# Kernel optimization log

Measured on AMD Instinct MI355X. Metric: run time of the kernel, lower is better.

The kernel has to match this reference:

```python
import jax, jax.numpy as jnp
import numpy as np

B, N1, N2, C = 4, 1024, 128, 1152
H, D = 16, 72            # num_heads, head_dim (1152 = 16*72)
HID = 4608               # mlp hidden = 4*1152
ATTN_SCALE = D ** -0.5
RMS_SCALE = C ** 0.5     # quirk: RMSNorm built with dim=1152 though applied over d=72
LN_EPS = 1e-6


def setup_inputs() -> dict:
    key = jax.random.key(0)
    ks = iter(jax.random.split(key, 64))
    n = lambda shape, s=1.0: jax.random.normal(next(ks), shape, jnp.float32) * s
    W = 0.02  # weight init scale
    inp = {
        "x": n((B, N1, C)),
        "c": n((B, N2, C)),
        "global_c": n((B, C)),
        "ada_x_w": n((C, 6 * C), W), "ada_x_b": jnp.zeros((6 * C,)),
        "ada_c_w": n((C, 6 * C), W), "ada_c_b": jnp.zeros((6 * C,)),
        "g1x_g": jnp.ones((C,)), "g1x_b": jnp.zeros((C,)),
        "g2x_g": jnp.ones((C,)), "g2x_b": jnp.zeros((C,)),
        "g1c_g": jnp.ones((C,)), "g1c_b": jnp.zeros((C,)),
        "g2c_g": jnp.ones((C,)), "g2c_b": jnp.zeros((C,)),
        "qkv_x_w": n((C, 3 * C), W), "qkv_x_b": jnp.zeros((3 * C,)),
        "proj_x_w": n((C, C), W), "proj_x_b": jnp.zeros((C,)),
        "qkv_c_w": n((C, 3 * C), W), "qkv_c_b": jnp.zeros((3 * C,)),
        "proj_c_w": n((C, C), W), "proj_c_b": jnp.zeros((C,)),
        "gq_x": jnp.ones((1,)), "gk_x": jnp.ones((1,)),
        "gq_c": jnp.ones((1,)), "gk_c": jnp.ones((1,)),
        "mlp_x_w1": n((C, HID), W), "mlp_x_b1": jnp.zeros((HID,)),
        "mlp_x_w2": n((HID, C), W), "mlp_x_b2": jnp.zeros((C,)),
        "mlp_c_w1": n((C, HID), W), "mlp_c_b1": jnp.zeros((HID,)),
        "mlp_c_w2": n((HID, C), W), "mlp_c_b2": jnp.zeros((C,)),
    }
    return inp


def _ln(t, g, b):
    m = t.mean(-1, keepdims=True)
    v = ((t - m) ** 2).mean(-1, keepdims=True)
    return (t - m) * jax.lax.rsqrt(v + LN_EPS) * g + b


def _modulate(t, shift, scale):  # shift/scale: [B, C]
    return t * (1.0 + scale[:, None, :]) + shift[:, None, :]


def _rms(t, g):  # F.normalize over last dim, then * sqrt(1152) * g
    nrm = jnp.sqrt(jnp.sum(t * t, axis=-1, keepdims=True))
    return t / jnp.maximum(nrm, 1e-12) * (RMS_SCALE * g)


def _heads(t):  # [B, N, H*D] -> [B, H, N, D]
    Bq, Nq, _ = t.shape
    return t.reshape(Bq, Nq, H, D).transpose(0, 2, 1, 3)


def _mmdit_forward(x, c, global_c,
                   ada_x_w, ada_x_b, ada_c_w, ada_c_b,
                   g1x_g, g1x_b, g2x_g, g2x_b, g1c_g, g1c_b, g2c_g, g2c_b,
                   qkv_x_w, qkv_x_b, proj_x_w, proj_x_b,
                   qkv_c_w, qkv_c_b, proj_c_w, proj_c_b,
                   gq_x, gk_x, gq_c, gk_c,
                   mlp_x_w1, mlp_x_b1, mlp_x_w2, mlp_x_b2,
                   mlp_c_w1, mlp_c_b1, mlp_c_w2, mlp_c_b2):
    s = jax.nn.silu(global_c)
    mod_x = jnp.split(s @ ada_x_w + ada_x_b, 6, axis=-1)
    mod_c = jnp.split(s @ ada_c_w + ada_c_b, 6, axis=-1)
    (sh_msa_x, sc_msa_x, gt_msa_x, sh_mlp_x, sc_mlp_x, gt_mlp_x) = mod_x
    (sh_msa_c, sc_msa_c, gt_msa_c, sh_mlp_c, sc_mlp_c, gt_mlp_c) = mod_c

    xin = _modulate(_ln(x, g1x_g, g1x_b), sh_msa_x, sc_msa_x)
    cin = _modulate(_ln(c, g1c_g, g1c_b), sh_msa_c, sc_msa_c)

    qx, kx, vx = jnp.split(xin @ qkv_x_w + qkv_x_b, 3, axis=-1)
    qc, kc, vc = jnp.split(cin @ qkv_c_w + qkv_c_b, 3, axis=-1)
    qx, kx, vx = _heads(qx), _heads(kx), _heads(vx)
    qc, kc, vc = _heads(qc), _heads(kc), _heads(vc)
    qx, kx = _rms(qx, gq_x), _rms(kx, gk_x)
    qc, kc = _rms(qc, gq_c), _rms(kc, gk_c)

    q = jnp.concatenate([qx, qc], axis=2)  # [B,H,N1+N2,D]
    k = jnp.concatenate([kx, kc], axis=2)
    v = jnp.concatenate([vx, vc], axis=2)

    scores = jnp.einsum('bhnd,bhmd->bhnm', q, k) * ATTN_SCALE
    attn = jax.nn.softmax(scores, axis=-1)
    o = jnp.einsum('bhnm,bhmd->bhnd', attn, v)
    o = o.transpose(0, 2, 1, 3).reshape(B, N1 + N2, C)
    ox, oc = o[:, :N1], o[:, N1:]
    attn_x = ox @ proj_x_w + proj_x_b
    attn_c = oc @ proj_c_w + proj_c_b

    x = x + gt_msa_x[:, None, :] * attn_x
    c = c + gt_msa_c[:, None, :] * attn_c

    hx = _modulate(_ln(x, g2x_g, g2x_b), sh_mlp_x, sc_mlp_x)
    hx = jax.nn.gelu(hx @ mlp_x_w1 + mlp_x_b1, approximate=True) @ mlp_x_w2 + mlp_x_b2
    x = x + gt_mlp_x[:, None, :] * hx

    hc = _modulate(_ln(c, g2c_g, g2c_b), sh_mlp_c, sc_mlp_c)
    hc = jax.nn.gelu(hc @ mlp_c_w1 + mlp_c_b1, approximate=True) @ mlp_c_w2 + mlp_c_b2
    c = c + gt_mlp_c[:, None, :] * hc
    return x, c


def reference(x, c, global_c,
              ada_x_w, ada_x_b, ada_c_w, ada_c_b,
              g1x_g, g1x_b, g2x_g, g2x_b, g1c_g, g1c_b, g2c_g, g2c_b,
              qkv_x_w, qkv_x_b, proj_x_w, proj_x_b,
              qkv_c_w, qkv_c_b, proj_c_w, proj_c_b,
              gq_x, gk_x, gq_c, gk_c,
              mlp_x_w1, mlp_x_b1, mlp_x_w2, mlp_x_b2,
              mlp_c_w1, mlp_c_b1, mlp_c_w2, mlp_c_b2):
    return _mmdit_forward(x, c, global_c,
                          ada_x_w, ada_x_b, ada_c_w, ada_c_b,
                          g1x_g, g1x_b, g2x_g, g2x_b, g1c_g, g1c_b, g2c_g, g2c_b,
                          qkv_x_w, qkv_x_b, proj_x_w, proj_x_b,
                          qkv_c_w, qkv_c_b, proj_c_w, proj_c_b,
                          gq_x, gk_x, gq_c, gk_c,
                          mlp_x_w1, mlp_x_b1, mlp_x_w2, mlp_x_b2,
                          mlp_c_w1, mlp_c_b1, mlp_c_w2, mlp_c_b2)
```

## Files before the change

### kernel.cpp

```cpp
#include <hip/hip_runtime.h>

typedef unsigned short u16;
typedef unsigned int u32;
typedef __attribute__((ext_vector_type(8))) short bf16x8;
typedef __attribute__((ext_vector_type(4))) float f32x4;

#define MX_ 4096
#define NT_ 1152
#define C_  1152
#define DP_ 96
#define D_  72
#define H_  16
#define MT_ 4608

static __device__ __forceinline__ float b2f(u16 u){ union{u32 i; float f;} x; x.i=((u32)u)<<16; return x.f; }
static __device__ __forceinline__ u16 f2b(float f){ u32 i=__float_as_uint(f); return (u16)((i + 0x7FFFu + ((i>>16)&1u))>>16); }

static __device__ __forceinline__ void gl_lds16(const u16* g, u16* l){
  __builtin_amdgcn_global_load_lds((const __attribute__((address_space(1))) void*)g,
                                   (__attribute__((address_space(3))) void*)l, 16, 0, 0);
}

#define MFMA16(a,b,c) __builtin_amdgcn_mfma_f32_16x16x32_bf16(a,b,c,0,0,0)

struct TrArgs {
  const float* src[8]; u16* dst[8]; int K[8]; int N[8]; int start[9];
};

__global__ __launch_bounds__(256) void transpose_kernel(TrArgs a){
  int bx = blockIdx.x;
  int mi = 0;
  #pragma unroll
  for (int i = 0; i < 8; ++i) if (bx >= a.start[i+1]) mi = i+1;
  int t = bx - a.start[mi];
  int K = a.K[mi], N = a.N[mi];
  int ntk = K >> 5;
  int tk = t % ntk, tn = t / ntk;
  int k0 = tk*32, n0 = tn*32;
  __shared__ u16 lds[32][33];
  int c = threadIdx.x & 31, r = threadIdx.x >> 5;
  const float* src = a.src[mi];
  u16* dst = a.dst[mi];
  #pragma unroll
  for (int ii = 0; ii < 4; ++ii){
    int row = r + ii*8;
    lds[row][c] = f2b(src[(size_t)(k0+row)*N + n0 + c]);
  }
  __syncthreads();
  #pragma unroll
  for (int ii = 0; ii < 4; ++ii){
    int row = r + ii*8;
    dst[(size_t)(n0+row)*K + k0 + c] = lds[c][row];
  }
}

__global__ __launch_bounds__(256) void ada_kernel(const float* gc, const float* wx, const float* bx,
                                                  const float* wc, const float* bc,
                                                  float* mod_x, float* mod_c){
  __shared__ float s[4][C_];
  __shared__ float part[4][4][64];
  int tid = threadIdx.x;
  for (int i = tid; i < 4*C_; i += 256){
    float v = gc[i];
    s[i / C_][i % C_] = v / (1.f + __expf(-v));
  }
  __syncthreads();
  int jq = tid & 63;
  int kq = tid >> 6;
  int jg = blockIdx.x*64 + jq;
  int which = jg / 6912;
  int j = jg % 6912;
  const float* W = which ? wc : wx;
  float a0=0.f, a1=0.f, a2=0.f, a3=0.f;
  for (int k = kq*288; k < kq*288 + 288; ++k){
    float w = W[(size_t)k*6912 + j];
    a0 += s[0][k]*w; a1 += s[1][k]*w; a2 += s[2][k]*w; a3 += s[3][k]*w;
  }
  part[kq][0][jq]=a0; part[kq][1][jq]=a1; part[kq][2][jq]=a2; part[kq][3][jq]=a3;
  __syncthreads();
  if (kq == 0){
    float bb = (which ? bc : bx)[j];
    float* out = which ? mod_c : mod_x;
    #pragma unroll
    for (int b = 0; b < 4; ++b){
      out[(size_t)b*6912 + j] = part[0][b][jq] + part[1][b][jq] + part[2][b][jq] + part[3][b][jq] + bb;
    }
  }
}

__global__ __launch_bounds__(256) void ln_mod_kernel(
  const float* srcx, const float* srcc, const float* g, const float* bt,
  const float* gcn, const float* btc,
  const float* shx, const float* scx, const float* shc, const float* scc,
  u16* out)
{
  int m = blockIdx.x;
  bool isC = (m >= MX_);
  const float* src = isC ? srcc + (size_t)(m - MX_)*C_ : srcx + (size_t)m*C_;
  int bidx = isC ? ((m - MX_) >> 7) : (m >> 10);
  const float* gg = isC ? gcn : g;
  const float* bb = isC ? btc : bt;
  const float* sh = (isC ? shc : shx) + (size_t)bidx*6912;
  const float* sc = (isC ? scc : scx) + (size_t)bidx*6912;
  int tid = threadIdx.x;
  float lv[8];
  float sum = 0.f, sq = 0.f;
  if (tid < 144){
    float4 v0 = *(const float4*)(src + tid*8);
    float4 v1 = *(const float4*)(src + tid*8 + 4);
    lv[0]=v0.x; lv[1]=v0.y; lv[2]=v0.z; lv[3]=v0.w;
    lv[4]=v1.x; lv[5]=v1.y; lv[6]=v1.z; lv[7]=v1.w;
    #pragma unroll
    for (int j = 0; j < 8; ++j){ sum += lv[j]; sq += lv[j]*lv[j]; }
  }
  #pragma unroll
  for (int off = 1; off < 64; off <<= 1){ sum += __shfl_xor(sum, off); sq += __shfl_xor(sq, off); }
  __shared__ float rs[4], rq[4];
  int wave = tid >> 6, lane = tid & 63;
  if (lane == 0){ rs[wave] = sum; rq[wave] = sq; }
  __syncthreads();
  float S = rs[0]+rs[1]+rs[2]+rs[3];
  float Q = rq[0]+rq[1]+rq[2]+rq[3];
  float mean = S * (1.f/1152.f);
  float var  = Q * (1.f/1152.f) - mean*mean;
  float rstd = rsqrtf(var + 1e-6f);
  if (tid < 144){
    union { uint4 v; u16 s[8]; } o;
    #pragma unroll
    for (int j = 0; j < 8; ++j){
      int n = tid*8 + j;
      float val = (lv[j] - mean)*rstd*gg[n] + bb[n];
      val = val*(1.f + sc[n]) + sh[n];
      o.s[j] = f2b(val);
    }
    *(uint4*)(out + (size_t)m*C_ + tid*8) = o.v;
  }
}

__global__ __launch_bounds__(256) void reduce2_kernel(
  const float* p,
  const float* residx, const float* residc,
  const float* modx, const float* modc,
  const float* biasx, const float* biasc,
  float* outx, float* outc)
{
  for (int i4 = blockIdx.x*256 + threadIdx.x; i4 < MT_*288; i4 += gridDim.x*256){
    int m = i4 / 288, n4 = (i4 % 288)*4;
    bool isC = (m >= MX_);
    int bidx = isC ? ((m - MX_) >> 7) : (m >> 10);
    const float* gate  = (isC ? modc : modx) + (size_t)bidx*6912;
    const float* bias  = isC ? biasc : biasx;
    const float* resid = isC ? residc + (size_t)(m - MX_)*C_ : residx + (size_t)m*C_;
    float* o = isC ? outc + (size_t)(m - MX_)*C_ : outx + (size_t)m*C_;
    float4 a = *(const float4*)(p + (size_t)m*C_ + n4);
    float4 b = *(const float4*)(p + (size_t)(MT_ + m)*C_ + n4);
    float4 r = *(const float4*)(resid + n4);
    float4 ov;
    ov.x = r.x + gate[n4+0]*(a.x + b.x + bias[n4+0]);
    ov.y = r.y + gate[n4+1]*(a.y + b.y + bias[n4+1]);
    ov.z = r.z + gate[n4+2]*(a.z + b.z + bias[n4+2]);
    ov.w = r.w + gate[n4+3]*(a.w + b.w + bias[n4+3]);
    *(float4*)(o + n4) = ov;
  }
}

struct GemmArgs {
  const u16* A; int lda; int rowmap;
  const u16* BTx; const u16* BTc;
  const float* biasx; const float* biasc;
  void* outx; void* outc;
  const float* residx; const float* residc;
  const float* gatex; const float* gatec;
  int N, K, kLen;
};

static __device__ __forceinline__ int amap(int m, int rowmap){
  if (rowmap){
    if (m < MX_) return (m >> 10)*NT_ + (m & 1023);
    int mm = m - MX_;
    return (mm >> 7)*NT_ + 1024 + (mm & 127);
  }
  return m;
}

template<int EPI>
__global__ __launch_bounds__(256, 2) void gemm_kernel(GemmArgs g){
  __shared__ u16 As[128*64];
  __shared__ u16 Bs[128*64];
  int gx = gridDim.x, gy = gridDim.y;
  int nwg = gx*gy;
  int orig = blockIdx.y*gx + blockIdx.x;
  int q = nwg >> 3, r8 = nwg & 7;
  int xcd = orig & 7, wi = orig >> 3;
  int swz = (xcd < r8 ? xcd*(q+1) : r8*(q+1) + (xcd - r8)*q) + wi;
  int n0 = (swz % gx)*128, m0 = (swz / gx)*128;
  int kStart = blockIdx.z * g.kLen;
  bool isC = (m0 >= MX_);
  const u16* BT = isC ? g.BTc : g.BTx;
  int tid = threadIdx.x, wave = tid >> 6, lane = tid & 63;
  int lg = lane >> 4, lr = lane & 15;
  int wm = wave >> 1, wn = wave & 1;
  f32x4 acc[4][4] = {};

  const u16* Aaddr[4]; const u16* Baddr[4];
  #pragma unroll
  for (int i = 0; i < 4; ++i){
    int cb = (wave*4 + i)*64;
    int qq = cb + lane;
    int row = qq >> 3;
    int c16 = (qq & 7) ^ (row & 7);
    Aaddr[i] = g.A + (size_t)amap(m0 + row, g.rowmap)*g.lda + kStart + c16*8;
    Baddr[i] = BT + (size_t)(n0 + row)*g.K + kStart + c16*8;
  }
  for (int k0 = 0; k0 < g.kLen; k0 += 64){
    #pragma unroll
    for (int i = 0; i < 4; ++i){
      int cb = (wave*4 + i)*64;
      gl_lds16(Aaddr[i] + k0, As + cb*8);
      gl_lds16(Baddr[i] + k0, Bs + cb*8);
    }
    __syncthreads();
    #pragma unroll
    for (int kkI = 0; kkI < 2; ++kkI){
      bf16x8 af[4], bfr[4];
      #pragma unroll
      for (int mi = 0; mi < 4; ++mi){
        int row = wm*64 + mi*16 + lr;
        int c16 = (kkI*4 + lg) ^ (row & 7);
        af[mi] = *(const bf16x8*)&As[row*64 + c16*8];
      }
      #pragma unroll
      for (int ni = 0; ni < 4; ++ni){
        int row = wn*64 + ni*16 + lr;
        int c16 = (kkI*4 + lg) ^ (row & 7);
        bfr[ni] = *(const bf16x8*)&Bs[row*64 + c16*8];
      }
      #pragma unroll
      for (int mi = 0; mi < 4; ++mi)
        #pragma unroll
        for (int ni = 0; ni < 4; ++ni)
          acc[mi][ni] = MFMA16(af[mi], bfr[ni], acc[mi][ni]);
    }
    __syncthreads();
  }

  const float* bias  = isC ? g.biasc : g.biasx;
  const float* resid = isC ? g.residc : g.residx;
  void* out = isC ? g.outc : g.outx;
  const float* gate = nullptr;
  if (EPI == 2){
    int bidx = isC ? ((m0 - MX_) >> 7) : (m0 >> 10);
    gate = (isC ? g.gatec : g.gatex) + (size_t)bidx*6912;
  }
  int mbase = isC ? (m0 - MX_) : m0;
  float* pbase = nullptr;
  if (EPI == 3) pbase = (float*)g.outx + (size_t)blockIdx.z*MT_*C_;
  #pragma unroll
  for (int mi = 0; mi < 4; ++mi){
    #pragma unroll
    for (int r = 0; r < 4; ++r){
      #pragma unroll
      for (int ni = 0; ni < 4; ++ni){
        int n = n0 + wn*64 + ni*16 + lr;
        if (EPI == 3){
          size_t prow = (size_t)(m0 + wm*64 + mi*16 + lg*4 + r);
          pbase[prow*(size_t)g.N + n] = acc[mi][ni][r];
        } else {
          size_t orow = (size_t)(mbase + wm*64 + mi*16 + lg*4 + r);
          float v = acc[mi][ni][r] + bias[n];
          if (EPI == 1){
            float u = 0.7978845608028654f*(v + 0.044715f*v*v*v);
            v = 0.5f*v*(1.f + tanhf(u));
          }
          if (EPI == 2){
            v = resid[orow*(size_t)g.N + n] + gate[n]*v;
            ((float*)out)[orow*(size_t)g.N + n] = v;
          } else {
            ((u16*)out)[orow*(size_t)g.N + n] = f2b(v);
          }
        }
      }
    }
  }
}

__global__ __launch_bounds__(256) void rmshead_kernel(
  const u16* qkv, const float* gqx, const float* gkx, const float* gqc, const float* gkc,
  u16* qpad, u16* kpad, u16* vT)
{
  int tt = blockIdx.x, h = blockIdx.y, b = blockIdx.z;
  int t0 = tt*64;
  bool isC = (t0 >= 1024);
  size_t rowbase = isC ? (size_t)(MX_ + b*128 + (t0 - 1024)) : (size_t)(b*1024 + t0);
  __shared__ u16 sq[2][64][72];
  __shared__ u16 sv[64][72];
  __shared__ float nf[2][64];
  int tid = threadIdx.x;
  for (int s = tid; s < 1728; s += 256){
    int which = s / 576, rem = s % 576;
    int t = rem / 9, ch = rem % 9;
    uint4 v = *(const uint4*)(qkv + (rowbase + t)*3456 + which*C_ + h*D_ + ch*8);
    u16* dst = (which < 2) ? &sq[which][t][ch*8] : &sv[t][ch*8];
    *(uint4*)dst = v;
  }
  __syncthreads();
  {
    int row = tid >> 1, half = tid & 1;
    int which = row >> 6, t = row & 63;
    float ss = 0.f;
    for (int d = half*36; d < half*36 + 36; ++d){
      float v = b2f(sq[which][t][d]); ss += v*v;
    }
    ss += __shfl_xor(ss, 1);
    if (half == 0){
      const float* gp = (which == 0) ? (isC ? gqc : gqx) : (isC ? gkc : gkx);
      float f = 33.9411254970f * gp[0] / fmaxf(sqrtf(ss), 1e-12f);
      if (which == 0) f *= 0.11785113019775793f;
      nf[which][t] = f;
    }
  }
  __syncthreads();
  size_t obase = ((size_t)(b*H_ + h)*NT_ + t0) * DP_;
  for (int s = tid; s < 1536; s += 256){
    int which = s / 768, rem = s % 768;
    int t = rem / 12, ch = rem % 12;
    float f = nf[which][t];
    union { uint4 v; u16 e[8]; } o;
    #pragma unroll
    for (int j = 0; j < 8; ++j){
      int d = ch*8 + j;
      o.e[j] = (d < D_) ? f2b(b2f(sq[which][t][d]) * f) : (u16)0;
    }
    *(uint4*)((which == 0 ? qpad : kpad) + obase + (size_t)t*DP_ + ch*8) = o.v;
  }
  size_t vbase = (size_t)(b*H_ + h)*80*NT_;
  for (int s = tid; s < 576; s += 256){
    int d = s / 8, ch = s % 8;
    union { uint4 v; u16 e[8]; } o;
    #pragma unroll
    for (int j = 0; j < 8; ++j) o.e[j] = sv[ch*8 + j][d];
    *(uint4*)(vT + vbase + (size_t)d*NT_ + t0 + ch*8) = o.v;
  }
  for (int s = tid; s < 512; s += 256){
    int d = 72 + (s >> 6), t = s & 63;
    vT[vbase + (size_t)d*NT_ + t0 + t] = (d == 72) ? (u16)0x3F80 : (u16)0;
  }
}

__global__ __launch_bounds__(256, 4) void attn_kernel(
  const u16* qpad, const u16* kpad, const u16* vT, u16* O)
{
  __shared__ u16 Ps[4][16][40];
  int orig = blockIdx.x;
  int w = (orig & 7)*144 + (orig >> 3);
  int qtb = w % 18, hb = w / 18;
  int h = hb & 15, b = hb >> 4;
  int bh = b*H_ + h;
  int tid = threadIdx.x, wave = tid >> 6, lane = tid & 63;
  int lg = lane >> 4, lr = lane & 15;
  int q0 = qtb*64 + wave*16;

  const u16* qb = qpad + (size_t)bh*NT_*DP_;
  const u16* kb = kpad + (size_t)bh*NT_*DP_;
  const u16* vb = vT + (size_t)bh*80*NT_;

  bf16x8 qf[3];
  #pragma unroll
  for (int kk = 0; kk < 3; ++kk)
    qf[kk] = *(const bf16x8*)(qb + (size_t)(q0 + lr)*DP_ + kk*32 + lg*8);

  f32x4 acc[5] = {};
  float m0 = -1e30f;

  bf16x8 kfA[2][3], kfB[2][3], vf[5];
  auto LOADK = [&](bf16x8 (&kf)[2][3], int kvt){
    #pragma unroll
    for (int kt = 0; kt < 2; ++kt)
      #pragma unroll
      for (int kk = 0; kk < 3; ++kk)
        kf[kt][kk] = *(const bf16x8*)(kb + (size_t)(kvt*32 + kt*16 + lr)*DP_ + kk*32 + lg*8);
  };
  u16* prow = &Ps[wave][lr][0];

  auto TILE = [&](bf16x8 (&kf)[2][3], bf16x8 (&kfn)[2][3], int t){
    #pragma unroll
    for (int dc = 0; dc < 5; ++dc)
      vf[dc] = *(const bf16x8*)(vb + (size_t)(dc*16 + lr)*NT_ + t*32 + lg*8);
    if (t + 1 < 36) LOADK(kfn, t + 1);

    f32x4 st[2] = {};
    __builtin_amdgcn_s_setprio(1);
    #pragma unroll
    for (int kk = 0; kk < 3; ++kk){
      st[0] = MFMA16(kf[0][kk], qf[kk], st[0]);
      st[1] = MFMA16(kf[1][kk], qf[kk], st[1]);
    }
    __builtin_amdgcn_s_setprio(0);

    float pm0 = fmaxf(fmaxf(fmaxf(st[0][0], st[0][1]), fmaxf(st[0][2], st[0][3])),
                      fmaxf(fmaxf(st[1][0], st[1][1]), fmaxf(st[1][2], st[1][3])));
    if (!__all(pm0 - m0 <= 8.f)){
      float r0 = fmaxf(pm0, __shfl_xor(pm0, 16)); r0 = fmaxf(r0, __shfl_xor(r0, 32));
      float n0 = fmaxf(m0, r0);
      float f0 = __expf(m0 - n0);
      m0 = n0;
      #pragma unroll
      for (int dc = 0; dc < 5; ++dc)
        #pragma unroll
        for (int j = 0; j < 4; ++j) acc[dc][j] *= f0;
    }
    #pragma unroll
    for (int kt = 0; kt < 2; ++kt){
      u32 w0 = (u32)f2b(__expf(st[kt][0] - m0)) | ((u32)f2b(__expf(st[kt][1] - m0)) << 16);
      u32 w1 = (u32)f2b(__expf(st[kt][2] - m0)) | ((u32)f2b(__expf(st[kt][3] - m0)) << 16);
      uint2 pkd; pkd.x = w0; pkd.y = w1;
      *(uint2*)(prow + kt*16 + lg*4) = pkd;
    }
    asm volatile("s_waitcnt lgkmcnt(0)" ::: "memory");
    __builtin_amdgcn_sched_barrier(0);
    bf16x8 bp = *(const bf16x8*)(prow + lg*8);
    __builtin_amdgcn_s_setprio(1);
    #pragma unroll
    for (int dc = 0; dc < 5; ++dc)
      acc[dc] = MFMA16(vf[dc], bp, acc[dc]);
    __builtin_amdgcn_s_setprio(0);
  };

  LOADK(kfA, 0);
  for (int t2 = 0; t2 < 18; ++t2){
    TILE(kfA, kfB, 2*t2);
    TILE(kfB, kfA, 2*t2 + 1);
  }

  float l0 = __shfl(acc[4][0], 32 + lr);
  float rl0 = 1.f / l0;
  #pragma unroll
  for (int dc = 0; dc < 5; ++dc){
    if (dc < 4 || lg < 2){
      union { uint2 v; u16 e[4]; } o;
      #pragma unroll
      for (int j = 0; j < 4; ++j) o.e[j] = f2b(acc[dc][j] * rl0);
      int tok = q0 + lr;
      *(uint2*)(O + ((size_t)b*NT_ + tok)*C_ + h*D_ + dc*16 + lg*4) = o.v;
    }
  }
}

extern "C" void kernel_launch(void* const* d_in, const int* in_sizes, int n_in,
                              void* d_out, int out_size, void* d_ws, size_t ws_size,
                              hipStream_t stream)
{
  (void)in_sizes; (void)n_in; (void)out_size; (void)ws_size;
  const float* x        = (const float*)d_in[0];
  const float* c        = (const float*)d_in[1];
  const float* gc       = (const float*)d_in[2];
  const float* ada_x_w  = (const float*)d_in[3];
  const float* ada_x_b  = (const float*)d_in[4];
  const float* ada_c_w  = (const float*)d_in[5];
  const float* ada_c_b  = (const float*)d_in[6];
  const float* g1x_g    = (const float*)d_in[7];
  const float* g1x_b    = (const float*)d_in[8];
  const float* g2x_g    = (const float*)d_in[9];
  const float* g2x_b    = (const float*)d_in[10];
  const float* g1c_g    = (const float*)d_in[11];
  const float* g1c_b    = (const float*)d_in[12];
  const float* g2c_g    = (const float*)d_in[13];
  const float* g2c_b    = (const float*)d_in[14];
  const float* qkv_x_w  = (const float*)d_in[15];
  const float* qkv_x_b  = (const float*)d_in[16];
  const float* proj_x_w = (const float*)d_in[17];
  const float* proj_x_b = (const float*)d_in[18];
  const float* qkv_c_w  = (const float*)d_in[19];
  const float* qkv_c_b  = (const float*)d_in[20];
  const float* proj_c_w = (const float*)d_in[21];
  const float* proj_c_b = (const float*)d_in[22];
  const float* gq_x     = (const float*)d_in[23];
  const float* gk_x     = (const float*)d_in[24];
  const float* gq_c     = (const float*)d_in[25];
  const float* gk_c     = (const float*)d_in[26];
  const float* m_x_w1   = (const float*)d_in[27];
  const float* m_x_b1   = (const float*)d_in[28];
  const float* m_x_w2   = (const float*)d_in[29];
  const float* m_x_b2   = (const float*)d_in[30];
  const float* m_c_w1   = (const float*)d_in[31];
  const float* m_c_b1   = (const float*)d_in[32];
  const float* m_c_w2   = (const float*)d_in[33];
  const float* m_c_b2   = (const float*)d_in[34];
  float* out = (float*)d_out;

  char* ws = (char*)d_ws;
  size_t off = 0;
  auto alloc = [&](size_t bytes)->void*{ void* p = ws + off; off += (bytes + 255) & ~(size_t)255; return p; };
  u16* WTqx  = (u16*)alloc((size_t)3456*1152*2);
  u16* WTqc  = (u16*)alloc((size_t)3456*1152*2);
  u16* WTpx  = (u16*)alloc((size_t)1152*1152*2);
  u16* WTpc  = (u16*)alloc((size_t)1152*1152*2);
  u16* WTm1x = (u16*)alloc((size_t)4608*1152*2);
  u16* WTm2x = (u16*)alloc((size_t)1152*4608*2);
  u16* WTm1c = (u16*)alloc((size_t)4608*1152*2);
  u16* WTm2c = (u16*)alloc((size_t)1152*4608*2);
  float* mod_x = (float*)alloc((size_t)4*6912*4);
  float* mod_c = (float*)alloc((size_t)4*6912*4);
  u16* xin  = (u16*)alloc((size_t)4608*1152*2);
  u16* pool = (u16*)alloc((size_t)4608*4608*2);
  u16* qpad = (u16*)alloc((size_t)64*1152*96*2 + 4096);
  u16* kpad = (u16*)alloc((size_t)64*1152*96*2 + 4096);
  u16* vTb  = (u16*)alloc((size_t)64*80*1152*2 + 4096);
  u16* Obuf = (u16*)alloc((size_t)4*1152*1152*2);
  float* x1c1 = (float*)alloc((size_t)4608*1152*4);
  float* fc2p = (float*)qpad;

  {
    TrArgs ta;
    const float* srcs[8] = {qkv_x_w, qkv_c_w, proj_x_w, proj_c_w, m_x_w1, m_x_w2, m_c_w1, m_c_w2};
    u16* dsts[8]         = {WTqx, WTqc, WTpx, WTpc, WTm1x, WTm2x, WTm1c, WTm2c};
    int Ks[8] = {1152,1152,1152,1152,1152,4608,1152,4608};
    int Ns[8] = {3456,3456,1152,1152,4608,1152,4608,1152};
    int st = 0;
    for (int i = 0; i < 8; ++i){
      ta.src[i] = srcs[i]; ta.dst[i] = dsts[i]; ta.K[i] = Ks[i]; ta.N[i] = Ns[i];
      ta.start[i] = st; st += (Ks[i]/32)*(Ns[i]/32);
    }
    ta.start[8] = st;
    transpose_kernel<<<dim3(st), dim3(256), 0, stream>>>(ta);
  }
  ada_kernel<<<dim3(216), dim3(256), 0, stream>>>(gc, ada_x_w, ada_x_b, ada_c_w, ada_c_b, mod_x, mod_c);
  ln_mod_kernel<<<dim3(4608), dim3(256), 0, stream>>>(
      x, c, g1x_g, g1x_b, g1c_g, g1c_b,
      mod_x + 0, mod_x + 1152, mod_c + 0, mod_c + 1152, xin);
  {
    GemmArgs ga{};
    ga.A = xin; ga.lda = 1152; ga.rowmap = 0;
    ga.BTx = WTqx; ga.BTc = WTqc; ga.biasx = qkv_x_b; ga.biasc = qkv_c_b;
    ga.outx = pool; ga.outc = pool + (size_t)4096*3456;
    ga.N = 3456; ga.K = 1152; ga.kLen = 1152;
    gemm_kernel<0><<<dim3(27,36), dim3(256), 0, stream>>>(ga);
  }
  rmshead_kernel<<<dim3(18,16,4), dim3(256), 0, stream>>>(pool, gq_x, gk_x, gq_c, gk_c, qpad, kpad, vTb);
  attn_kernel<<<dim3(1152), dim3(256), 0, stream>>>(qpad, kpad, vTb, Obuf);
  {
    GemmArgs ga{};
    ga.A = Obuf; ga.lda = 1152; ga.rowmap = 1;
    ga.BTx = WTpx; ga.BTc = WTpc; ga.biasx = proj_x_b; ga.biasc = proj_c_b;
    ga.outx = x1c1; ga.outc = x1c1 + (size_t)4096*1152;
    ga.residx = x; ga.residc = c;
    ga.gatex = mod_x + 2*1152; ga.gatec = mod_c + 2*1152;
    ga.N = 1152; ga.K = 1152; ga.kLen = 1152;
    gemm_kernel<2><<<dim3(9,36), dim3(256), 0, stream>>>(ga);
  }
  ln_mod_kernel<<<dim3(4608), dim3(256), 0, stream>>>(
      x1c1, x1c1 + (size_t)4096*1152, g2x_g, g2x_b, g2c_g, g2c_b,
      mod_x + 3*1152, mod_x + 4*1152, mod_c + 3*1152, mod_c + 4*1152, xin);
  {
    GemmArgs ga{};
    ga.A = xin; ga.lda = 1152; ga.rowmap = 0;
    ga.BTx = WTm1x; ga.BTc = WTm1c; ga.biasx = m_x_b1; ga.biasc = m_c_b1;
    ga.outx = pool; ga.outc = pool + (size_t)4096*4608;
    ga.N = 4608; ga.K = 1152; ga.kLen = 1152;
    gemm_kernel<1><<<dim3(36,36), dim3(256), 0, stream>>>(ga);
  }
  {
    GemmArgs ga{};
    ga.A = pool; ga.lda = 4608; ga.rowmap = 0;
    ga.BTx = WTm2x; ga.BTc = WTm2c;
    ga.outx = fc2p;
    ga.N = 1152; ga.K = 4608; ga.kLen = 2304;
    gemm_kernel<3><<<dim3(9,36,2), dim3(256), 0, stream>>>(ga);
  }
  reduce2_kernel<<<dim3(2048), dim3(256), 0, stream>>>(
      fc2p, x1c1, x1c1 + (size_t)4096*1152,
      mod_x + 5*1152, mod_c + 5*1152, m_x_b2, m_c_b2,
      out, out + (size_t)4096*1152);
}
```

Before: 512.2 us.

## Stage K tiles in LDS shared across eight waves and use exp2 softmax

Attention blocks grow to 512 threads covering 128 queries, and K tiles are loaded once per block into swizzled, double-buffered LDS via direct global-to-LDS loads instead of each wave reading K from global memory. The log2(e) factor is folded into the Q scale so the softmax can use exp2, and P is packed to bf16 with a hardware convert instruction. K is stored with a padded 128-element row stride to suit the swizzle. The change adds a block-wide barrier every KV tile and enlarges the K buffer, which may reduce overlap and occupancy.

Result: faster. 485.0 us (-5.3%).

```diff
diff --git a/kernel.cpp b/kernel.cpp
--- a/kernel.cpp
+++ b/kernel.cpp
@@ -9,6 +9,7 @@
 #define NT_ 1152
 #define C_  1152
 #define DP_ 96
+#define DPK_ 128
 #define D_  72
 #define H_  16
 #define MT_ 4608
@@ -286,7 +287,7 @@
 
 __global__ __launch_bounds__(256) void rmshead_kernel(
   const u16* qkv, const float* gqx, const float* gkx, const float* gqc, const float* gkc,
-  u16* qpad, u16* kpad, u16* vT)
+  u16* qpad, u16* kpadp, u16* vT)
 {
   int tt = blockIdx.x, h = blockIdx.y, b = blockIdx.z;
   int t0 = tt*64;
@@ -315,23 +316,38 @@
     if (half == 0){
       const float* gp = (which == 0) ? (isC ? gqc : gqx) : (isC ? gkc : gkx);
       float f = 33.9411254970f * gp[0] / fmaxf(sqrtf(ss), 1e-12f);
-      if (which == 0) f *= 0.11785113019775793f;
+      if (which == 0) f *= 0.17002324581205f;
       nf[which][t] = f;
     }
   }
   __syncthreads();
-  size_t obase = ((size_t)(b*H_ + h)*NT_ + t0) * DP_;
-  for (int s = tid; s < 1536; s += 256){
-    int which = s / 768, rem = s % 768;
-    int t = rem / 12, ch = rem % 12;
-    float f = nf[which][t];
+  size_t obaseQ = ((size_t)(b*H_ + h)*NT_ + t0) * DP_;
+  for (int s = tid; s < 768; s += 256){
+    int t = s / 12, ch = s % 12;
+    float f = nf[0][t];
     union { uint4 v; u16 e[8]; } o;
     #pragma unroll
     for (int j = 0; j < 8; ++j){
       int d = ch*8 + j;
-      o.e[j] = (d < D_) ? f2b(b2f(sq[which][t][d]) * f) : (u16)0;
-    }
-    *(uint4*)((which == 0 ? qpad : kpad) + obase + (size_t)t*DP_ + ch*8) = o.v;
+      o.e[j] = (d < D_) ? f2b(b2f(sq[0][t][d]) * f) : (u16)0;
+    }
+    *(uint4*)(qpad + obaseQ + (size_t)t*DP_ + ch*8) = o.v;
+  }
+  size_t obaseK = ((size_t)(b*H_ + h)*NT_ + t0) * DPK_;
+  for (int s = tid; s < 1024; s += 256){
+    int t = s >> 4, ch = s & 15;
+    union { uint4 v; u16 e[8]; } o;
+    if (ch < 9){
+      float f = nf[1][t];
+      #pragma unroll
+      for (int j = 0; j < 8; ++j){
+        int d = ch*8 + j;
+        o.e[j] = (d < D_) ? f2b(b2f(sq[1][t][d]) * f) : (u16)0;
+      }
+    } else {
+      o.v = make_uint4(0,0,0,0);
+    }
+    *(uint4*)(kpadp + obaseK + (size_t)t*DPK_ + ch*8) = o.v;
   }
   size_t vbase = (size_t)(b*H_ + h)*80*NT_;
   for (int s = tid; s < 576; s += 256){
@@ -347,21 +363,22 @@
   }
 }
 
-__global__ __launch_bounds__(256, 4) void attn_kernel(
-  const u16* qpad, const u16* kpad, const u16* vT, u16* O)
+__global__ __launch_bounds__(512) void attn_kernel(
+  const u16* qpad, const u16* kpadp, const u16* vT, u16* O)
 {
-  __shared__ u16 Ps[4][16][40];
+  __shared__ u16 Ks[2][32*DPK_];
+  __shared__ u16 Ps[8][16][40];
   int orig = blockIdx.x;
-  int w = (orig & 7)*144 + (orig >> 3);
-  int qtb = w % 18, hb = w / 18;
+  int w = (orig & 7)*72 + (orig >> 3);
+  int qtb = w % 9, hb = w / 9;
   int h = hb & 15, b = hb >> 4;
   int bh = b*H_ + h;
   int tid = threadIdx.x, wave = tid >> 6, lane = tid & 63;
   int lg = lane >> 4, lr = lane & 15;
-  int q0 = qtb*64 + wave*16;
+  int q0 = qtb*128 + wave*16;
 
   const u16* qb = qpad + (size_t)bh*NT_*DP_;
-  const u16* kb = kpad + (size_t)bh*NT_*DP_;
+  const u16* kb = kpadp + (size_t)bh*NT_*DPK_;
   const u16* vb = vT + (size_t)bh*80*NT_;
 
   bf16x8 qf[3];
@@ -372,21 +389,40 @@
   f32x4 acc[5] = {};
   float m0 = -1e30f;
 
-  bf16x8 kfA[2][3], kfB[2][3], vf[5];
-  auto LOADK = [&](bf16x8 (&kf)[2][3], int kvt){
-    #pragma unroll
-    for (int kt = 0; kt < 2; ++kt)
-      #pragma unroll
-      for (int kk = 0; kk < 3; ++kk)
-        kf[kt][kk] = *(const bf16x8*)(kb + (size_t)(kvt*32 + kt*16 + lr)*DP_ + kk*32 + lg*8);
+  int srow = wave*4 + (lane >> 4);
+  int schunk = (lane & 15) ^ (srow & 7);
+  const u16* ksrc = kb + (size_t)srow*DPK_ + schunk*8;
+  u16* kdst0 = &Ks[0][(wave*4)*DPK_];
+  u16* kdst1 = &Ks[1][(wave*4)*DPK_];
+
+  auto STAGEK = [&](int buf, int kvt){
+    gl_lds16(ksrc + (size_t)kvt*32*DPK_, buf ? kdst1 : kdst0);
   };
+
   u16* prow = &Ps[wave][lr][0];
-
-  auto TILE = [&](bf16x8 (&kf)[2][3], bf16x8 (&kfn)[2][3], int t){
+  bf16x8 vf[5];
+
+  STAGEK(0, 0);
+  asm volatile("s_waitcnt vmcnt(0)" ::: "memory");
+  __syncthreads();
+
+  for (int t = 0; t < 36; ++t){
+    int buf = t & 1;
     #pragma unroll
     for (int dc = 0; dc < 5; ++dc)
       vf[dc] = *(const bf16x8*)(vb + (size_t)(dc*16 + lr)*NT_ + t*32 + lg*8);
-    if (t + 1 < 36) LOADK(kfn, t + 1);
+    if (t + 1 < 36) STAGEK(buf ^ 1, t + 1);
+
+    const u16* kbase = &Ks[buf][0];
+    bf16x8 kf[2][3];
+    #pragma unroll
+    for (int kt = 0; kt < 2; ++kt)
+      #pragma unroll
+      for (int kk = 0; kk < 3; ++kk){
+        int row = kt*16 + lr;
+        int ch  = (kk*4 + lg) ^ (lr & 7);
+        kf[kt][kk] = *(const bf16x8*)&kbase[row*DPK_ + ch*8];
+      }
 
     f32x4 st[2] = {};
     __builtin_amdgcn_s_setprio(1);
@@ -399,10 +435,10 @@
 
     float pm0 = fmaxf(fmaxf(fmaxf(st[0][0], st[0][1]), fmaxf(st[0][2], st[0][3])),
                       fmaxf(fmaxf(st[1][0], st[1][1]), fmaxf(st[1][2], st[1][3])));
-    if (!__all(pm0 - m0 <= 8.f)){
+    if (!__all(pm0 - m0 <= 11.5415603f)){
       float r0 = fmaxf(pm0, __shfl_xor(pm0, 16)); r0 = fmaxf(r0, __shfl_xor(r0, 32));
       float n0 = fmaxf(m0, r0);
-      float f0 = __expf(m0 - n0);
+      float f0 = exp2f(m0 - n0);
       m0 = n0;
       #pragma unroll
       for (int dc = 0; dc < 5; ++dc)
@@ -411,9 +447,14 @@
     }
     #pragma unroll
     for (int kt = 0; kt < 2; ++kt){
-      u32 w0 = (u32)f2b(__expf(st[kt][0] - m0)) | ((u32)f2b(__expf(st[kt][1] - m0)) << 16);
-      u32 w1 = (u32)f2b(__expf(st[kt][2] - m0)) | ((u32)f2b(__expf(st[kt][3] - m0)) << 16);
-      uint2 pkd; pkd.x = w0; pkd.y = w1;
+      float e0 = exp2f(st[kt][0] - m0);
+      float e1 = exp2f(st[kt][1] - m0);
+      float e2 = exp2f(st[kt][2] - m0);
+      float e3 = exp2f(st[kt][3] - m0);
+      u32 lo, hi;
+      asm("v_cvt_pk_bf16_f32 %0, %1, %2" : "=v"(lo) : "v"(e0), "v"(e1));
+      asm("v_cvt_pk_bf16_f32 %0, %1, %2" : "=v"(hi) : "v"(e2), "v"(e3));
+      uint2 pkd; pkd.x = lo; pkd.y = hi;
       *(uint2*)(prow + kt*16 + lg*4) = pkd;
     }
     asm volatile("s_waitcnt lgkmcnt(0)" ::: "memory");
@@ -424,12 +465,9 @@
     for (int dc = 0; dc < 5; ++dc)
       acc[dc] = MFMA16(vf[dc], bp, acc[dc]);
     __builtin_amdgcn_s_setprio(0);
-  };
-
-  LOADK(kfA, 0);
-  for (int t2 = 0; t2 < 18; ++t2){
-    TILE(kfA, kfB, 2*t2);
-    TILE(kfB, kfA, 2*t2 + 1);
+
+    asm volatile("s_waitcnt vmcnt(0)" ::: "memory");
+    __syncthreads();
   }
 
   float l0 = __shfl(acc[4][0], 32 + lr);
@@ -504,7 +542,7 @@
   u16* xin  = (u16*)alloc((size_t)4608*1152*2);
   u16* pool = (u16*)alloc((size_t)4608*4608*2);
   u16* qpad = (u16*)alloc((size_t)64*1152*96*2 + 4096);
-  u16* kpad = (u16*)alloc((size_t)64*1152*96*2 + 4096);
+  u16* kpadp= (u16*)alloc((size_t)64*1152*128*2 + 4096);
   u16* vTb  = (u16*)alloc((size_t)64*80*1152*2 + 4096);
   u16* Obuf = (u16*)alloc((size_t)4*1152*1152*2);
   float* x1c1 = (float*)alloc((size_t)4608*1152*4);
@@ -536,8 +574,8 @@
     ga.N = 3456; ga.K = 1152; ga.kLen = 1152;
     gemm_kernel<0><<<dim3(27,36), dim3(256), 0, stream>>>(ga);
   }
-  rmshead_kernel<<<dim3(18,16,4), dim3(256), 0, stream>>>(pool, gq_x, gk_x, gq_c, gk_c, qpad, kpad, vTb);
-  attn_kernel<<<dim3(1152), dim3(256), 0, stream>>>(qpad, kpad, vTb, Obuf);
+  rmshead_kernel<<<dim3(18,16,4), dim3(256), 0, stream>>>(pool, gq_x, gk_x, gq_c, gk_c, qpad, kpadp, vTb);
+  attn_kernel<<<dim3(576), dim3(512), 0, stream>>>(qpad, kpadp, vTb, Obuf);
   {
     GemmArgs ga{};
     ga.A = Obuf; ga.lda = 1152; ga.rowmap = 1;
```
